# Kernel optimization log

Hardware: AMD Instinct MI355X
Metric: run time of the kernel (lower is better)

## Reference

```python
import jax, jax.numpy as jnp
from jax import lax
import numpy as np

B, T, I, H, O = 128, 256, 256, 1024, 128


def _rnn_layer(x, W_ih, W_hh, b_ih, b_hh):
    # x: [B, T, D_in] -> hidden states [B, T, H]
    # precompute input projection for all timesteps (batched GEMM)
    xW = jnp.einsum('btd,hd->bth', x, W_ih) + b_ih + b_hh  # [B, T, H]

    def step(h, xw_t):
        h = jnp.tanh(xw_t + h @ W_hh.T)  # [B, H]
        return h, h

    h0 = jnp.zeros((x.shape[0], W_hh.shape[0]), x.dtype)
    _, hs = lax.scan(step, h0, jnp.swapaxes(xW, 0, 1))  # hs: [T, B, H]
    return jnp.swapaxes(hs, 0, 1)  # [B, T, H]


def setup_inputs() -> dict:
    key = jax.random.key(0)
    ks = jax.random.split(key, 11)
    s_ih0 = 1.0 / np.sqrt(H)
    inp = {
        'X': jax.random.normal(ks[0], (B, T, I), jnp.float32),
        'W_ih0': jax.random.uniform(ks[1], (H, I), jnp.float32, -s_ih0, s_ih0),
        'W_hh0': jax.random.uniform(ks[2], (H, H), jnp.float32, -s_ih0, s_ih0),
        'b_ih0': jax.random.uniform(ks[3], (H,), jnp.float32, -s_ih0, s_ih0),
        'b_hh0': jax.random.uniform(ks[4], (H,), jnp.float32, -s_ih0, s_ih0),
        'W_ih1': jax.random.uniform(ks[5], (H, H), jnp.float32, -s_ih0, s_ih0),
        'W_hh1': jax.random.uniform(ks[6], (H, H), jnp.float32, -s_ih0, s_ih0),
        'b_ih1': jax.random.uniform(ks[7], (H,), jnp.float32, -s_ih0, s_ih0),
        'b_hh1': jax.random.uniform(ks[8], (H,), jnp.float32, -s_ih0, s_ih0),
        'W_fc': jax.random.uniform(ks[9], (O, H), jnp.float32, -s_ih0, s_ih0),
        'b_fc': jax.random.uniform(ks[10], (O,), jnp.float32, -s_ih0, s_ih0),
    }
    return inp


def reference(X, W_ih0, W_hh0, b_ih0, b_hh0, W_ih1, W_hh1, b_ih1, b_hh1, W_fc, b_fc):
    h1 = _rnn_layer(X, W_ih0, W_hh0, b_ih0, b_hh0)   # layer 0: [B, T, H]
    h2 = _rnn_layer(h1, W_ih1, W_hh1, b_ih1, b_hh1)  # layer 1: [B, T, H]
    last = h2[:, -1, :]                               # [B, H]
    return last @ W_fc.T + b_fc                       # [B, O]
```

## Files before the change

### kernel.cpp

```cpp
#include <hip/hip_runtime.h>
#include <stdint.h>
#include <stddef.h>

#define B_ 128
#define T_ 256
#define I_ 256
#define H_ 1024
#define O_ 128

typedef __attribute__((ext_vector_type(8))) __bf16 bf16x8;
typedef __attribute__((ext_vector_type(4))) float f32x4;
typedef unsigned long long u64;



__global__ void split_kernel(const float* __restrict__ src, __bf16* __restrict__ hi,
                             __bf16* __restrict__ lo, int n) {
    int i = blockIdx.x * blockDim.x + threadIdx.x;
    int stride = gridDim.x * blockDim.x;
    for (; i < n; i += stride) {
        float v = src[i];
        __bf16 h = (__bf16)v;
        hi[i] = h;
        lo[i] = (__bf16)(v - (float)h);
    }
}

__global__ void pack_x(const float* __restrict__ X, __bf16* __restrict__ xh,
                       __bf16* __restrict__ xl) {
    int i = blockIdx.x * 256 + threadIdx.x;
    int lnidx = i & 15;
    int kg   = (i >> 4) & 31;
    int bgrp = (i >> 9) & 7;
    int t    = i >> 12;
    int b = bgrp * 16 + lnidx;
    const float* xs = X + (long)b * T_ * I_ + (long)t * I_ + kg * 8;
    float4 f0 = *(const float4*)xs;
    float4 f1 = *(const float4*)(xs + 4);
    float f[8] = {f0.x, f0.y, f0.z, f0.w, f1.x, f1.y, f1.z, f1.w};
    bf16x8 hv, lv;
    #pragma unroll
    for (int j = 0; j < 8; ++j) {
        __bf16 h = (__bf16)f[j];
        hv[j] = h;
        lv[j] = (__bf16)(f[j] - (float)h);
    }
    long o = (long)t * 32768 + (long)(bgrp * 32 + kg) * 128 + lnidx * 8;
    *(bf16x8*)(xh + o) = hv;
    *(bf16x8*)(xl + o) = lv;
}

__global__ void bias_sum_kernel(const float* __restrict__ a, const float* __restrict__ b,
                                float* __restrict__ o, int n) {
    int i = blockIdx.x * blockDim.x + threadIdx.x;
    if (i < n) o[i] = a[i] + b[i];
}

__global__ void transpose_fc(const float* __restrict__ w, float* __restrict__ wt) {
    int i = blockIdx.x * blockDim.x + threadIdx.x;
    if (i < O_ * H_) {
        int o = i / H_, k = i - o * H_;
        wt[k * O_ + o] = w[i];
    }
}

union Frag { u64 d[2]; bf16x8 v; };

template <int CPW, int SEG0CH, bool CACHED0>
__device__ __forceinline__ void step_full(
    const __bf16* __restrict__ A0h, const __bf16* __restrict__ A0l,
    const __bf16* __restrict__ Sh,  const __bf16* __restrict__ Sl,
    const bf16x8 (&wh)[CPW][2], const bf16x8 (&wl)[CPW][2],
    const float* __restrict__ bs,
    __bf16* __restrict__ Soh, __bf16* __restrict__ Sol,
    int bt, int jt, int w, float* red)
{
    const int lane = threadIdx.x & 63;
    const int ln = lane & 15;
    const int q  = lane >> 4;

    f32x4 acc[2][2][2];
    #pragma unroll
    for (int s = 0; s < 2; ++s)
        #pragma unroll
        for (int n = 0; n < 2; ++n)
            #pragma unroll
            for (int r = 0; r < 2; ++r)
                acc[s][n][r] = (f32x4){0.f, 0.f, 0.f, 0.f};

    Frag SH[2][2], SL[2][2];

    auto issue = [&](int c, Frag (&FH)[2], Frag (&FL)[2]) {
        const int gC = w * CPW + c;
        if (gC < SEG0CH) {
            #pragma unroll
            for (int s = 0; s < 2; ++s) {
                long off = ((long)(bt * 2 + s) * (SEG0CH * 4) + gC * 4 + q) * 128 + ln * 8;
                if constexpr (CACHED0) {
                    FH[s].v = *(const bf16x8*)(A0h + off);
                    FL[s].v = *(const bf16x8*)(A0l + off);
                } else {
                    const u64* ph = (const u64*)(A0h + off);
                    const u64* pl = (const u64*)(A0l + off);
                    FH[s].d[0] = __hip_atomic_load(ph,     __ATOMIC_RELAXED, __HIP_MEMORY_SCOPE_AGENT);
                    FH[s].d[1] = __hip_atomic_load(ph + 1, __ATOMIC_RELAXED, __HIP_MEMORY_SCOPE_AGENT);
                    FL[s].d[0] = __hip_atomic_load(pl,     __ATOMIC_RELAXED, __HIP_MEMORY_SCOPE_AGENT);
                    FL[s].d[1] = __hip_atomic_load(pl + 1, __ATOMIC_RELAXED, __HIP_MEMORY_SCOPE_AGENT);
                }
            }
        } else {
            #pragma unroll
            for (int s = 0; s < 2; ++s) {
                long off = ((long)(bt * 2 + s) * 128 + (gC - SEG0CH) * 4 + q) * 128 + ln * 8;
                const u64* ph = (const u64*)(Sh + off);
                const u64* pl = (const u64*)(Sl + off);
                FH[s].d[0] = __hip_atomic_load(ph,     __ATOMIC_RELAXED, __HIP_MEMORY_SCOPE_AGENT);
                FH[s].d[1] = __hip_atomic_load(ph + 1, __ATOMIC_RELAXED, __HIP_MEMORY_SCOPE_AGENT);
                FL[s].d[0] = __hip_atomic_load(pl,     __ATOMIC_RELAXED, __HIP_MEMORY_SCOPE_AGENT);
                FL[s].d[1] = __hip_atomic_load(pl + 1, __ATOMIC_RELAXED, __HIP_MEMORY_SCOPE_AGENT);
            }
        }
    };

    issue(0, SH[0], SL[0]);
    issue(1, SH[1], SL[1]);

    #pragma unroll
    for (int c = 0; c < CPW; ++c) {
        bf16x8 ah[2], al[2];
        #pragma unroll
        for (int s = 0; s < 2; ++s) { ah[s] = SH[c & 1][s].v; al[s] = SL[c & 1][s].v; }
        if (c + 2 < CPW) issue(c + 2, SH[c & 1], SL[c & 1]);
        #pragma unroll
        for (int s = 0; s < 2; ++s)
            #pragma unroll
            for (int n = 0; n < 2; ++n) {
                acc[s][n][0] = __builtin_amdgcn_mfma_f32_16x16x32_bf16(ah[s], wh[c][n], acc[s][n][0], 0, 0, 0);
                acc[s][n][1] = __builtin_amdgcn_mfma_f32_16x16x32_bf16(al[s], wh[c][n], acc[s][n][1], 0, 0, 0);
                acc[s][n][1] = __builtin_amdgcn_mfma_f32_16x16x32_bf16(ah[s], wl[c][n], acc[s][n][1], 0, 0, 0);
            }
    }

    {
        float* my = red + w * 1056;
        #pragma unroll
        for (int s = 0; s < 2; ++s)
            #pragma unroll
            for (int n = 0; n < 2; ++n) {
                f32x4 sum = acc[s][n][0] + acc[s][n][1];
                #pragma unroll
                for (int r = 0; r < 4; ++r)
                    my[(s * 16 + q * 4 + r) * 33 + n * 16 + ln] = sum[r];
            }
    }
    __syncthreads();

    {
        int tid = threadIdx.x;
        int row = tid & 31;
        int jp  = tid >> 5;
        int c0 = jp * 2;
        float v0 = 0.f, v1 = 0.f;
        #pragma unroll
        for (int w8 = 0; w8 < 8; ++w8) {
            v0 += red[w8 * 1056 + row * 33 + c0];
            v1 += red[w8 * 1056 + row * 33 + c0 + 1];
        }
        int j0 = jt * 32 + c0;
        float h0 = tanhf(v0 + bs[j0]);
        float h1v = tanhf(v1 + bs[j0 + 1]);
        union { __bf16 b; unsigned short u; } x0h, x0l, x1h, x1l;
        x0h.b = (__bf16)h0;  x0l.b = (__bf16)(h0 - (float)x0h.b);
        x1h.b = (__bf16)h1v; x1l.b = (__bf16)(h1v - (float)x1h.b);
        unsigned uh = (unsigned)x0h.u | ((unsigned)x1h.u << 16);
        unsigned ul = (unsigned)x0l.u | ((unsigned)x1l.u << 16);
        long idx = ((long)(bt * 2 + (row >> 4)) * 128 + jt * 4 + (c0 >> 3)) * 128
                 + (row & 15) * 8 + (c0 & 7);
        __hip_atomic_store((unsigned*)(Soh + idx), uh, __ATOMIC_RELAXED, __HIP_MEMORY_SCOPE_AGENT);
        __hip_atomic_store((unsigned*)(Sol + idx), ul, __ATOMIC_RELAXED, __HIP_MEMORY_SCOPE_AGENT);
    }
}

__device__ __forceinline__ void bar_arrive(unsigned* bar, int slot, unsigned k) {
    asm volatile("s_waitcnt vmcnt(0)" ::: "memory");
    __syncthreads();
    if (threadIdx.x == 0) {
        unsigned old = __hip_atomic_fetch_add(&bar[slot * 64], 1u, __ATOMIC_RELAXED,
                                              __HIP_MEMORY_SCOPE_AGENT);
        if (old == k * 32u + 31u)
            __hip_atomic_store(&bar[slot * 64 + 32], k + 1u, __ATOMIC_RELAXED,
                               __HIP_MEMORY_SCOPE_AGENT);
    }
}

__device__ __forceinline__ void bar_wait(unsigned* bar, int slot, unsigned v) {
    if (threadIdx.x == 0) {
        while (__hip_atomic_load(&bar[slot * 64 + 32], __ATOMIC_RELAXED,
                                 __HIP_MEMORY_SCOPE_AGENT) < v)
            __builtin_amdgcn_s_sleep(2);
    }
    __syncthreads();
    asm volatile("" ::: "memory");
}

struct PArgs {
    const __bf16 *xh, *xl;
    const __bf16 *Wi0h, *Wi0l, *Wr0h, *Wr0l;
    const __bf16 *Wi1h, *Wi1l, *Wr1h, *Wr1l;
    const float *bs0, *bs1;
    __bf16 *s0ah, *s0al, *s0bh, *s0bl;
    __bf16 *s1ah, *s1al, *s1bh, *s1bl;
    unsigned* bar;
};

__global__ __launch_bounds__(512, 2) void persistent_rnn(PArgs a) {
    __shared__ float red[8 * 1056];
    const int w = threadIdx.x >> 6;
    const int lane = threadIdx.x & 63;
    const int ln = lane & 15;
    const int q  = lane >> 4;
    const int layer = blockIdx.x >> 7;
    const int r7 = blockIdx.x & 127;
    const int jt = r7 & 31;
    const int bt = r7 >> 5;
    const int slotL0 = 0 * 4 + bt;
    const int slotL1 = 1 * 4 + bt;

    if (layer == 0) {
        bf16x8 wh[5][2], wl[5][2];
        #pragma unroll
        for (int c = 0; c < 5; ++c) {
            int gC = w * 5 + c;
            #pragma unroll
            for (int n = 0; n < 2; ++n) {
                int jr = jt * 32 + n * 16 + ln;
                if (gC < 8) {
                    wh[c][n] = *(const bf16x8*)(a.Wi0h + (long)jr * 256 + gC * 32 + q * 8);
                    wl[c][n] = *(const bf16x8*)(a.Wi0l + (long)jr * 256 + gC * 32 + q * 8);
                } else {
                    wh[c][n] = *(const bf16x8*)(a.Wr0h + (long)jr * 1024 + (gC - 8) * 32 + q * 8);
                    wl[c][n] = *(const bf16x8*)(a.Wr0l + (long)jr * 1024 + (gC - 8) * 32 + q * 8);
                }
            }
        }
        for (int t = 0; t < T_; ++t) {
            const __bf16* sinh_ = (t & 1) ? a.s0bh : a.s0ah;
            const __bf16* sinl_ = (t & 1) ? a.s0bl : a.s0al;
            __bf16* south      = (t & 1) ? a.s0ah : a.s0bh;
            __bf16* soutl      = (t & 1) ? a.s0al : a.s0bl;
            if (t >= 1) bar_wait(a.bar, slotL0, (unsigned)t);
            if (t >= 2) bar_wait(a.bar, slotL1, (unsigned)(t - 1));
            step_full<5, 8, true>(a.xh + (long)t * 32768, a.xl + (long)t * 32768,
                                  sinh_, sinl_, wh, wl, a.bs0,
                                  south, soutl, bt, jt, w, red);
            bar_arrive(a.bar, slotL0, (unsigned)t);
        }
    } else {
        bf16x8 wh[8][2], wl[8][2];
        #pragma unroll
        for (int c = 0; c < 8; ++c) {
            int gC = w * 8 + c;
            #pragma unroll
            for (int n = 0; n < 2; ++n) {
                int jr = jt * 32 + n * 16 + ln;
                if (gC < 32) {
                    wh[c][n] = *(const bf16x8*)(a.Wi1h + (long)jr * 1024 + gC * 32 + q * 8);
                    wl[c][n] = *(const bf16x8*)(a.Wi1l + (long)jr * 1024 + gC * 32 + q * 8);
                } else {
                    wh[c][n] = *(const bf16x8*)(a.Wr1h + (long)jr * 1024 + (gC - 32) * 32 + q * 8);
                    wl[c][n] = *(const bf16x8*)(a.Wr1l + (long)jr * 1024 + (gC - 32) * 32 + q * 8);
                }
            }
        }
        for (int r = 1; r <= T_; ++r) {
            int t1 = r - 1;
            const __bf16* h1h = (t1 & 1) ? a.s0ah : a.s0bh;
            const __bf16* h1l = (t1 & 1) ? a.s0al : a.s0bl;
            const __bf16* sinh_ = (t1 & 1) ? a.s1bh : a.s1ah;
            const __bf16* sinl_ = (t1 & 1) ? a.s1bl : a.s1al;
            __bf16* south       = (t1 & 1) ? a.s1ah : a.s1bh;
            __bf16* soutl       = (t1 & 1) ? a.s1al : a.s1bl;
            bar_wait(a.bar, slotL0, (unsigned)r);
            if (r >= 2) bar_wait(a.bar, slotL1, (unsigned)(r - 1));
            step_full<8, 32, false>(h1h, h1l, sinh_, sinl_, wh, wl, a.bs1,
                                    south, soutl, bt, jt, w, red);
            bar_arrive(a.bar, slotL1, (unsigned)(r - 1));
        }
    }
}

__global__ __launch_bounds__(128) void fc_kernel(const __bf16* __restrict__ sph,
                                                 const __bf16* __restrict__ spl,
                                                 const float* __restrict__ wt,
                                                 const float* __restrict__ bfc,
                                                 float* __restrict__ out) {
    int b = blockIdx.x;
    int o = threadIdx.x;
    float acc = 0.f;
    #pragma unroll 2
    for (int kg = 0; kg < 128; ++kg) {
        long off = ((long)(b >> 4) * 128 + kg) * 128 + (b & 15) * 8;
        bf16x8 hv = *(const bf16x8*)(sph + off);
        bf16x8 lv = *(const bf16x8*)(spl + off);
        #pragma unroll
        for (int j = 0; j < 8; ++j) {
            float x = (float)hv[j] + (float)lv[j];
            acc += x * wt[(kg * 8 + j) * O_ + o];
        }
    }
    out[b * O_ + o] = acc + bfc[o];
}


extern "C" void kernel_launch(void* const* d_in, const int* in_sizes, int n_in,
                              void* d_out, int out_size, void* d_ws, size_t ws_size,
                              hipStream_t stream) {
    const float* X     = (const float*)d_in[0];
    const float* Wih0  = (const float*)d_in[1];
    const float* Whh0  = (const float*)d_in[2];
    const float* bih0  = (const float*)d_in[3];
    const float* bhh0  = (const float*)d_in[4];
    const float* Wih1  = (const float*)d_in[5];
    const float* Whh1  = (const float*)d_in[6];
    const float* bih1  = (const float*)d_in[7];
    const float* bhh1  = (const float*)d_in[8];
    const float* Wfc   = (const float*)d_in[9];
    const float* bfc   = (const float*)d_in[10];
    float* out = (float*)d_out;

    char* p = (char*)d_ws;
    auto alloc = [&](size_t bytes) -> void* {
        void* r = (void*)p;
        p += (bytes + 255) & ~(size_t)255;
        return r;
    };
    const size_t nW0 = (size_t)H_ * I_;
    const size_t nW  = (size_t)H_ * H_;
    const size_t planeSt = (size_t)131072;
    __bf16* xh   = (__bf16*)alloc((size_t)T_ * 32768 * 2);
    __bf16* xl   = (__bf16*)alloc((size_t)T_ * 32768 * 2);
    __bf16* W0h  = (__bf16*)alloc(nW0 * 2);
    __bf16* W0l  = (__bf16*)alloc(nW0 * 2);
    __bf16* Wh0h = (__bf16*)alloc(nW * 2);
    __bf16* Wh0l = (__bf16*)alloc(nW * 2);
    __bf16* Wi1h = (__bf16*)alloc(nW * 2);
    __bf16* Wi1l = (__bf16*)alloc(nW * 2);
    __bf16* Wh1h = (__bf16*)alloc(nW * 2);
    __bf16* Wh1l = (__bf16*)alloc(nW * 2);
    __bf16* s0ah = (__bf16*)alloc(planeSt * 2);
    __bf16* s0al = (__bf16*)alloc(planeSt * 2);
    __bf16* s0bh = (__bf16*)alloc(planeSt * 2);
    __bf16* s0bl = (__bf16*)alloc(planeSt * 2);
    __bf16* s1ah = (__bf16*)alloc(planeSt * 2);
    __bf16* s1al = (__bf16*)alloc(planeSt * 2);
    __bf16* s1bh = (__bf16*)alloc(planeSt * 2);
    __bf16* s1bl = (__bf16*)alloc(planeSt * 2);
    float* wfct = (float*)alloc((size_t)H_ * O_ * 4);
    float* bs0  = (float*)alloc((size_t)H_ * 4);
    float* bs1  = (float*)alloc((size_t)H_ * 4);
    unsigned* bar = (unsigned*)alloc(4096);
    (void)ws_size; (void)n_in; (void)in_sizes; (void)out_size;

    pack_x<<<4096, 256, 0, stream>>>(X, xh, xl);
    split_kernel<<<512, 256, 0, stream>>>(Wih0, W0h, W0l, (int)nW0);
    split_kernel<<<1024, 256, 0, stream>>>(Whh0, Wh0h, Wh0l, (int)nW);
    split_kernel<<<1024, 256, 0, stream>>>(Wih1, Wi1h, Wi1l, (int)nW);
    split_kernel<<<1024, 256, 0, stream>>>(Whh1, Wh1h, Wh1l, (int)nW);
    bias_sum_kernel<<<4, 256, 0, stream>>>(bih0, bhh0, bs0, H_);
    bias_sum_kernel<<<4, 256, 0, stream>>>(bih1, bhh1, bs1, H_);
    transpose_fc<<<(O_ * H_ + 255) / 256, 256, 0, stream>>>(Wfc, wfct);

    hipMemsetAsync(s0ah, 0, planeSt * 2, stream);
    hipMemsetAsync(s0al, 0, planeSt * 2, stream);
    hipMemsetAsync(s1ah, 0, planeSt * 2, stream);
    hipMemsetAsync(s1al, 0, planeSt * 2, stream);
    hipMemsetAsync(bar, 0, 4096, stream);

    PArgs args;
    args.xh = xh; args.xl = xl;
    args.Wi0h = W0h; args.Wi0l = W0l; args.Wr0h = Wh0h; args.Wr0l = Wh0l;
    args.Wi1h = Wi1h; args.Wi1l = Wi1l; args.Wr1h = Wh1h; args.Wr1l = Wh1l;
    args.bs0 = bs0; args.bs1 = bs1;
    args.s0ah = s0ah; args.s0al = s0al; args.s0bh = s0bh; args.s0bl = s0bl;
    args.s1ah = s1ah; args.s1al = s1al; args.s1bh = s1bh; args.s1bl = s1bl;
    args.bar = bar;
    void* kp[] = { &args };
    hipLaunchCooperativeKernel((void*)persistent_rnn, dim3(256), dim3(512), kp, 0, stream);

    fc_kernel<<<B_, O_, 0, stream>>>(s1ah, s1al, wfct, bfc, out);
}
```

Measured before the change: 2.265 ms.

## Replace block-wide barrier waits with per-wave dependency waits in persistent RNN

```diff
diff --git a/kernel.cpp b/kernel.cpp
--- a/kernel.cpp
+++ b/kernel.cpp
@@ -64,6 +64,26 @@
     }
 }
 
+
+__device__ __forceinline__ void wave_wait(unsigned* bar, int slot, unsigned v) {
+    while (__hip_atomic_load(&bar[slot * 64 + 32], __ATOMIC_RELAXED,
+                             __HIP_MEMORY_SCOPE_AGENT) < v)
+        __builtin_amdgcn_s_sleep(1);
+    asm volatile("" ::: "memory");
+}
+
+__device__ __forceinline__ void bar_arrive(unsigned* bar, int slot, unsigned k) {
+    asm volatile("s_waitcnt vmcnt(0)" ::: "memory");
+    __syncthreads();
+    if (threadIdx.x == 0) {
+        unsigned old = __hip_atomic_fetch_add(&bar[slot * 64], 1u, __ATOMIC_RELAXED,
+                                              __HIP_MEMORY_SCOPE_AGENT);
+        if (old == k * 32u + 31u)
+            __hip_atomic_store(&bar[slot * 64 + 32], k + 1u, __ATOMIC_RELAXED,
+                               __HIP_MEMORY_SCOPE_AGENT);
+    }
+}
+
 union Frag { u64 d[2]; bf16x8 v; };
 
 template <int CPW, int SEG0CH, bool CACHED0>
@@ -73,11 +93,15 @@
     const bf16x8 (&wh)[CPW][2], const bf16x8 (&wl)[CPW][2],
     const float* __restrict__ bs,
     __bf16* __restrict__ Soh, __bf16* __restrict__ Sol,
-    int bt, int jt, int w, float* red)
+    int bt, int jt, int w, float* red,
+    unsigned* bar, int ldSlot, unsigned ldVal,
+    int epSlotA, unsigned epValA, int epSlotB, unsigned epValB)
 {
     const int lane = threadIdx.x & 63;
     const int ln = lane & 15;
     const int q  = lane >> 4;
+
+    wave_wait(bar, ldSlot, ldVal);
 
     f32x4 acc[2][2][2];
     #pragma unroll
@@ -155,10 +179,13 @@
     }
     __syncthreads();
 
+    wave_wait(bar, epSlotA, epValA);
+    wave_wait(bar, epSlotB, epValB);
+
     {
         int tid = threadIdx.x;
-        int row = tid & 31;
-        int jp  = tid >> 5;
+        int row = tid >> 4;
+        int jp  = tid & 15;
         int c0 = jp * 2;
         float v0 = 0.f, v1 = 0.f;
         #pragma unroll
@@ -181,28 +208,6 @@
     }
 }
 
-__device__ __forceinline__ void bar_arrive(unsigned* bar, int slot, unsigned k) {
-    asm volatile("s_waitcnt vmcnt(0)" ::: "memory");
-    __syncthreads();
-    if (threadIdx.x == 0) {
-        unsigned old = __hip_atomic_fetch_add(&bar[slot * 64], 1u, __ATOMIC_RELAXED,
-                                              __HIP_MEMORY_SCOPE_AGENT);
-        if (old == k * 32u + 31u)
-            __hip_atomic_store(&bar[slot * 64 + 32], k + 1u, __ATOMIC_RELAXED,
-                               __HIP_MEMORY_SCOPE_AGENT);
-    }
-}
-
-__device__ __forceinline__ void bar_wait(unsigned* bar, int slot, unsigned v) {
-    if (threadIdx.x == 0) {
-        while (__hip_atomic_load(&bar[slot * 64 + 32], __ATOMIC_RELAXED,
-                                 __HIP_MEMORY_SCOPE_AGENT) < v)
-            __builtin_amdgcn_s_sleep(2);
-    }
-    __syncthreads();
-    asm volatile("" ::: "memory");
-}
-
 struct PArgs {
     const __bf16 *xh, *xl;
     const __bf16 *Wi0h, *Wi0l, *Wr0h, *Wr0l;
@@ -248,11 +253,13 @@
             const __bf16* sinl_ = (t & 1) ? a.s0bl : a.s0al;
             __bf16* south      = (t & 1) ? a.s0ah : a.s0bh;
             __bf16* soutl      = (t & 1) ? a.s0al : a.s0bl;
-            if (t >= 1) bar_wait(a.bar, slotL0, (unsigned)t);
-            if (t >= 2) bar_wait(a.bar, slotL1, (unsigned)(t - 1));
+            unsigned ldVal = (w >= 1) ? (unsigned)t : 0u;
             step_full<5, 8, true>(a.xh + (long)t * 32768, a.xl + (long)t * 32768,
                                   sinh_, sinl_, wh, wl, a.bs0,
-                                  south, soutl, bt, jt, w, red);
+                                  south, soutl, bt, jt, w, red,
+                                  a.bar, slotL0, ldVal,
+                                  slotL0, (w == 0) ? (unsigned)t : 0u,
+                                  slotL1, (t >= 1) ? (unsigned)(t - 1) : 0u);
             bar_arrive(a.bar, slotL0, (unsigned)t);
         }
     } else {
@@ -280,10 +287,14 @@
             const __bf16* sinl_ = (t1 & 1) ? a.s1bl : a.s1al;
             __bf16* south       = (t1 & 1) ? a.s1ah : a.s1bh;
             __bf16* soutl       = (t1 & 1) ? a.s1al : a.s1bl;
-            bar_wait(a.bar, slotL0, (unsigned)r);
-            if (r >= 2) bar_wait(a.bar, slotL1, (unsigned)(r - 1));
+            int ldSlot       = (w < 4) ? slotL0 : slotL1;
+            unsigned ldVal   = (w < 4) ? (unsigned)r
+                                       : ((r >= 2) ? (unsigned)(r - 1) : 0u);
             step_full<8, 32, false>(h1h, h1l, sinh_, sinl_, wh, wl, a.bs1,
-                                    south, soutl, bt, jt, w, red);
+                                    south, soutl, bt, jt, w, red,
+                                    a.bar, ldSlot, ldVal,
+                                    slotL1, (r >= 2) ? (unsigned)(r - 1) : 0u,
+                                    slotL1, 0u);
             bar_arrive(a.bar, slotL1, (unsigned)(r - 1));
         }
     }
```

After: 2.282 ms. Within noise of the previous version (+0.7%).
